# Kernel tuning notes

Measured on AMD Instinct MI355X. Metric: run time of the kernel, lower is better.

Reference implementation:

```python
import jax, jax.numpy as jnp
import numpy as np
import math

DIM = 512
HEADS = 8
DIM_HEAD = 64
SCALE = math.sqrt(DIM_HEAD)
EPS = 1e-12


def rms_norm(x, g):
    # F.normalize(x, dim=1) * g * sqrt(dim); x: [B, C, H, W], g: [C]
    inv = jax.lax.rsqrt(jnp.sum(x * x, axis=1, keepdims=True) + EPS)
    return x * inv * g[None, :, None, None] * jnp.asarray(math.sqrt(x.shape[1]), x.dtype)


def setup_inputs() -> dict:
    key = jax.random.key(0)
    k1, k2, k3 = jax.random.split(key, 3)
    B, H, W = 8, 64, 64
    hidden = HEADS * DIM_HEAD
    x = jax.random.normal(k1, (B, DIM, H, W), dtype=jnp.float32)
    w_qkv = jax.random.normal(k2, (3 * hidden, DIM), dtype=jnp.float32) * (1.0 / math.sqrt(DIM))
    w_out = jax.random.normal(k3, (DIM, hidden), dtype=jnp.float32) * (1.0 / math.sqrt(hidden))
    b_out = jnp.zeros((DIM,), dtype=jnp.float32)
    g1 = jnp.ones((DIM,), dtype=jnp.float32)
    g2 = jnp.ones((DIM,), dtype=jnp.float32)
    return {"x": x, "g1": g1, "w_qkv": w_qkv, "w_out": w_out, "b_out": b_out, "g2": g2}


def reference(x, g1, w_qkv, w_out, b_out, g2):
    B, C, H, W = x.shape
    n = H * W
    xn = rms_norm(x, g1)
    # 1x1 conv == channel matmul: [B, 3*hidden, H, W]
    qkv = jnp.einsum('bchw,oc->bohw', xn, w_qkv)
    q, k, v = jnp.split(qkv, 3, axis=1)
    # b (h c) x y -> b h c n
    def to_heads(t):
        return t.reshape(B, HEADS, DIM_HEAD, n)
    q, k, v = to_heads(q), to_heads(k), to_heads(v)
    q = jax.nn.softmax(q, axis=2) / SCALE   # softmax over channel dim d
    k = jax.nn.softmax(k, axis=3)           # softmax over spatial dim n
    context = jnp.einsum('bhdn,bhen->bhde', k, v)   # [B, H, d, e]
    out = jnp.einsum('bhde,bhdn->bhen', context, q) # [B, H, e, n]
    out = out.reshape(B, HEADS * DIM_HEAD, H, W)
    out = jnp.einsum('bchw,oc->bohw', out, w_out) + b_out[None, :, None, None]
    return rms_norm(out, g2)
```

## Files before the change

kernel.cpp:

```cpp
#include <hip/hip_runtime.h>


typedef unsigned short u16;
typedef __attribute__((ext_vector_type(8))) short short8;
typedef __attribute__((ext_vector_type(4))) short short4_t;
typedef __attribute__((ext_vector_type(4))) float f32x4;

static constexpr size_t XN_B = (size_t)512 * 4096;
static constexpr size_t KV_B = (size_t)1024 * 4096;
static constexpr float SQRT512 = 22.62741699796952f;

typedef const __attribute__((address_space(1))) unsigned int gu32;
typedef __attribute__((address_space(3))) unsigned int lu32;

__device__ __forceinline__ float b2f(u16 u){
  union { unsigned u; float f; } x; x.u = ((unsigned)u) << 16; return x.f;
}
__device__ __forceinline__ u16 f2b(float f){
  union { float f; unsigned u; } x; x.f = f;
  unsigned r = x.u + 0x7FFFu + ((x.u >> 16) & 1u);
  return (u16)(r >> 16);
}
__device__ __forceinline__ void gl16(const u16* g, u16* l){
  __builtin_amdgcn_global_load_lds((gu32*)g, (lu32*)l, 16, 0, 0);
}

__global__ __launch_bounds__(256)
void kprep(const float* __restrict__ wqkv, const float* __restrict__ wout,
           const float* __restrict__ g1, u16* __restrict__ dq, u16* __restrict__ dw,
           const float* __restrict__ x, u16* __restrict__ xnT,
           float* __restrict__ sden){
  __shared__ u16 lt[32][514];
  __shared__ float red4[256][4];
  __shared__ float invs[32];
  int bid = blockIdx.x;
  int t = threadIdx.x;
  if (bid < 1024){
    if (bid < 16) sden[bid * 256 + t] = 0.f;
    size_t i = ((size_t)bid * 256 + t) * 4;
    short4_t o;
    if (i < (size_t)786432){
      f32x4 v = *(const f32x4*)(wqkv + i);
      int c = (int)(i & 511);
      #pragma unroll
      for (int j = 0; j < 4; j++) o[j] = (short)f2b(v[j] * g1[c + j] * SQRT512);
      *(short4_t*)(dq + i) = o;
    } else {
      size_t off = i - 786432;
      f32x4 v = *(const f32x4*)(wout + off);
      #pragma unroll
      for (int j = 0; j < 4; j++) o[j] = (short)f2b(v[j]);
      *(short4_t*)(dw + off) = o;
    }
    return;
  }
  int pg0 = (bid - 1024) * 32;
  int b = pg0 >> 12, p0 = pg0 & 4095;
  int pxg = (t & 7) * 4;
  int chunk = t >> 3;
  const float* xp = x + (size_t)b * XN_B + p0 + pxg;
  f32x4 s = {0.f, 0.f, 0.f, 0.f};
  #pragma unroll 4
  for (int c = chunk * 16; c < chunk * 16 + 16; ++c){
    f32x4 v = *(const f32x4*)(xp + (size_t)c * 4096);
    #pragma unroll
    for (int j = 0; j < 4; j++){
      lt[pxg + j][c] = f2b(v[j]);
      s[j] += v[j] * v[j];
    }
  }
  *(f32x4*)red4[t] = s;
  __syncthreads();
  if (t < 32){
    int pg = t >> 2, pe = t & 3;
    float sum = 0.f;
    #pragma unroll
    for (int ch = 0; ch < 32; ch++) sum += red4[ch * 8 + pg][pe];
    invs[t] = rsqrtf(sum + 1e-12f);
  }
  __syncthreads();
  int px2 = t >> 3, c0 = (t & 7) * 8;
  float iv = invs[px2];
  u16* dst = xnT + (size_t)(pg0 + px2) * 512;
  #pragma unroll
  for (int j = 0; j < 8; j++){
    int c = c0 + j * 64;
    short8 o;
    #pragma unroll
    for (int e = 0; e < 8; e++) o[e] = (short)f2b(b2f(lt[px2][c + e]) * iv);
    *(short8*)(dst + c) = o;
  }
}

__global__ __launch_bounds__(256)
void gemm_qkv(const u16* __restrict__ Wkv, const u16* __restrict__ wq,
              const u16* __restrict__ xnT, u16* __restrict__ kvb,
              u16* __restrict__ qT)
{
  constexpr int NT = 8;
  const int bid = blockIdx.x;
  const u16* A; const u16* BT; u16* C;
  int m0, n0; size_t ldc; bool smax;
  if (bid < 2048){
    int ntile = bid & 31, mtile = (bid >> 5) & 7, z = bid >> 8;
    A = Wkv; BT = xnT + (size_t)z * XN_B; C = kvb + (size_t)z * KV_B;
    m0 = mtile * 128; n0 = ntile * 128; ldc = 4096; smax = false;
  } else {
    int idx = bid - 2048;
    int ntile = idx & 3, mtile = idx >> 2;
    A = xnT; BT = wq; C = qT;
    m0 = mtile * 128; n0 = ntile * 128; ldc = 512; smax = true;
  }
  __shared__ u16 As[2][128 * 64];
  __shared__ u16 Bs[2][128 * 64];
  const int tid = threadIdx.x;
  const int srow0 = tid >> 3;
  const int schunk = tid & 7;
  const int lane = tid & 63, wid = tid >> 6;
  const int wr = (wid >> 1) * 64, wc = (wid & 1) * 64;
  const int fr = lane & 15, fq = lane >> 4;
  f32x4 acc[4][4] = {};

  auto STAGE = [&](int s, int t){
    const int k0 = t * 64;
    #pragma unroll
    for (int r = 0; r < 4; r++){
      int row = r * 32 + srow0;
      int gj = (schunk ^ (row & 7)) * 8;
      gl16(A  + (size_t)(m0 + row) * 512 + k0 + gj, &As[s][0] + r * 2048 + tid * 8);
      gl16(BT + (size_t)(n0 + row) * 512 + k0 + gj, &Bs[s][0] + r * 2048 + tid * 8);
    }
  };

  STAGE(0, 0);
  int cur = 0;
  for (int t = 0; t < NT; t++){
    if (t + 1 < NT){
      STAGE(cur ^ 1, t + 1);
      asm volatile("s_waitcnt vmcnt(8)" ::: "memory");
    } else {
      asm volatile("s_waitcnt vmcnt(0)" ::: "memory");
    }
    __builtin_amdgcn_s_barrier();
    __builtin_amdgcn_sched_barrier(0);
    #pragma unroll
    for (int ks = 0; ks < 2; ks++){
      short8 a[4], b[4];
      #pragma unroll
      for (int i = 0; i < 4; i++){
        int ra = wr + i * 16 + fr;
        a[i] = *(const short8*)(&As[cur][0] + ra * 64 + ((ks * 4 + fq) ^ (ra & 7)) * 8);
        int rb = wc + i * 16 + fr;
        b[i] = *(const short8*)(&Bs[cur][0] + rb * 64 + ((ks * 4 + fq) ^ (rb & 7)) * 8);
      }
      #pragma unroll
      for (int i = 0; i < 4; i++)
        #pragma unroll
        for (int j = 0; j < 4; j++)
          acc[i][j] = __builtin_amdgcn_mfma_f32_16x16x32_bf16(a[i], b[j], acc[i][j], 0, 0, 0);
    }
    __builtin_amdgcn_sched_barrier(0);
    __builtin_amdgcn_s_barrier();
    cur ^= 1;
  }

  if (smax){
    #pragma unroll
    for (int i = 0; i < 4; i++)
      #pragma unroll
      for (int e = 0; e < 4; e++){
        float mx = fmaxf(fmaxf(acc[i][0][e], acc[i][1][e]),
                         fmaxf(acc[i][2][e], acc[i][3][e]));
        mx = fmaxf(mx, __shfl_xor(mx, 1));
        mx = fmaxf(mx, __shfl_xor(mx, 2));
        mx = fmaxf(mx, __shfl_xor(mx, 4));
        mx = fmaxf(mx, __shfl_xor(mx, 8));
        float p0 = __expf(acc[i][0][e] - mx);
        float p1 = __expf(acc[i][1][e] - mx);
        float p2 = __expf(acc[i][2][e] - mx);
        float p3 = __expf(acc[i][3][e] - mx);
        float s = p0 + p1 + p2 + p3;
        s += __shfl_xor(s, 1);
        s += __shfl_xor(s, 2);
        s += __shfl_xor(s, 4);
        s += __shfl_xor(s, 8);
        float r = 1.f / (s * 8.0f);
        acc[i][0][e] = p0 * r; acc[i][1][e] = p1 * r;
        acc[i][2][e] = p2 * r; acc[i][3][e] = p3 * r;
      }
  }
  #pragma unroll
  for (int i = 0; i < 4; i++)
    #pragma unroll
    for (int j = 0; j < 4; j++)
      #pragma unroll
      for (int e = 0; e < 4; e++){
        int row = m0 + wr + i * 16 + fq * 4 + e;
        int col = n0 + wc + j * 16 + fr;
        C[(size_t)row * ldc + col] = f2b(acc[i][j][e]);
      }
}

__global__ __launch_bounds__(256)
void gemm_out(const u16* __restrict__ qT, const u16* __restrict__ Mb,
              u16* __restrict__ out2T, const float* __restrict__ bias)
{
  constexpr int NT = 8;
  const int z = blockIdx.z;
  const u16* A  = qT + (size_t)z * 4096 * 512;
  const u16* BT = Mb + (size_t)z * 262144;
  u16* C = out2T + (size_t)z * 4096 * 512;
  const int m0 = blockIdx.y * 128, n0 = blockIdx.x * 128;
  __shared__ u16 As[2][128 * 64];
  __shared__ u16 Bs[2][128 * 64];
  const int tid = threadIdx.x;
  const int srow0 = tid >> 3;
  const int schunk = tid & 7;
  const int lane = tid & 63, wid = tid >> 6;
  const int wr = (wid >> 1) * 64, wc = (wid & 1) * 64;
  const int fr = lane & 15, fq = lane >> 4;
  f32x4 acc[4][4] = {};

  auto STAGE = [&](int s, int t){
    const int k0 = t * 64;
    #pragma unroll
    for (int r = 0; r < 4; r++){
      int row = r * 32 + srow0;
      int gj = (schunk ^ (row & 7)) * 8;
      gl16(A  + (size_t)(m0 + row) * 512 + k0 + gj, &As[s][0] + r * 2048 + tid * 8);
      gl16(BT + (size_t)(n0 + row) * 512 + k0 + gj, &Bs[s][0] + r * 2048 + tid * 8);
    }
  };

  STAGE(0, 0);
  int cur = 0;
  for (int t = 0; t < NT; t++){
    if (t + 1 < NT){
      STAGE(cur ^ 1, t + 1);
      asm volatile("s_waitcnt vmcnt(8)" ::: "memory");
    } else {
      asm volatile("s_waitcnt vmcnt(0)" ::: "memory");
    }
    __builtin_amdgcn_s_barrier();
    __builtin_amdgcn_sched_barrier(0);
    #pragma unroll
    for (int ks = 0; ks < 2; ks++){
      short8 a[4], b[4];
      #pragma unroll
      for (int i = 0; i < 4; i++){
        int ra = wr + i * 16 + fr;
        a[i] = *(const short8*)(&As[cur][0] + ra * 64 + ((ks * 4 + fq) ^ (ra & 7)) * 8);
        int rb = wc + i * 16 + fr;
        b[i] = *(const short8*)(&Bs[cur][0] + rb * 64 + ((ks * 4 + fq) ^ (rb & 7)) * 8);
      }
      #pragma unroll
      for (int i = 0; i < 4; i++)
        #pragma unroll
        for (int j = 0; j < 4; j++)
          acc[i][j] = __builtin_amdgcn_mfma_f32_16x16x32_bf16(a[i], b[j], acc[i][j], 0, 0, 0);
    }
    __builtin_amdgcn_sched_barrier(0);
    __builtin_amdgcn_s_barrier();
    cur ^= 1;
  }

  #pragma unroll
  for (int i = 0; i < 4; i++)
    #pragma unroll
    for (int j = 0; j < 4; j++)
      #pragma unroll
      for (int e = 0; e < 4; e++){
        int row = m0 + wr + i * 16 + fq * 4 + e;
        int col = n0 + wc + j * 16 + fr;
        C[(size_t)row * 512 + col] = f2b(acc[i][j][e] + bias[col]);
      }
}

__global__ __launch_bounds__(256)
void gemm_ctx(const u16* __restrict__ kv, float* __restrict__ P,
              float* __restrict__ sden)
{
  constexpr int K = 512;
  const int z = blockIdx.z;
  const int tid = threadIdx.x;
  const int ar = tid >> 2, ac = (tid & 3) * 8;
  int bh = z >> 3, sp = z & 7, b = bh >> 3, h = bh & 7;
  const u16* A  = kv + (size_t)b * KV_B + (size_t)(h * 64) * 4096 + sp * 512;
  const u16* BT = kv + (size_t)b * KV_B + (size_t)(512 + h * 64) * 4096 + sp * 512;
  __shared__ u16 As[64 * 40];
  __shared__ u16 Bs[64 * 40];
  const int wid = tid >> 6, lane = tid & 63;
  const int wr = (wid >> 1) * 32, wc = (wid & 1) * 32;
  const int lr = lane & 15, kb = lane >> 4;
  f32x4 acc[2][2] = {};
  float ssum = 0.f;
  for (int k0 = 0; k0 < K; k0 += 32){
    short8 av = *(const short8*)(A + (size_t)ar * 4096 + k0 + ac);
    short8 ao;
    #pragma unroll
    for (int e = 0; e < 8; e++){
      float ev = __expf(b2f((u16)av[e]));
      ao[e] = (short)f2b(ev);
      ssum += ev;
    }
    *(short8*)(As + ar * 40 + ac) = ao;
    *(short8*)(Bs + ar * 40 + ac) = *(const short8*)(BT + (size_t)ar * 4096 + k0 + ac);
    __syncthreads();
    short8 a0 = *(const short8*)(As + (wr +      lr) * 40 + kb * 8);
    short8 a1 = *(const short8*)(As + (wr + 16 + lr) * 40 + kb * 8);
    short8 b0 = *(const short8*)(Bs + (wc +      lr) * 40 + kb * 8);
    short8 b1 = *(const short8*)(Bs + (wc + 16 + lr) * 40 + kb * 8);
    acc[0][0] = __builtin_amdgcn_mfma_f32_16x16x32_bf16(a0, b0, acc[0][0], 0, 0, 0);
    acc[0][1] = __builtin_amdgcn_mfma_f32_16x16x32_bf16(a0, b1, acc[0][1], 0, 0, 0);
    acc[1][0] = __builtin_amdgcn_mfma_f32_16x16x32_bf16(a1, b0, acc[1][0], 0, 0, 0);
    acc[1][1] = __builtin_amdgcn_mfma_f32_16x16x32_bf16(a1, b1, acc[1][1], 0, 0, 0);
    __syncthreads();
  }
  ssum += __shfl_xor(ssum, 1);
  ssum += __shfl_xor(ssum, 2);
  if ((tid & 3) == 0) atomicAdd(sden + b * 512 + h * 64 + ar, ssum);
  #pragma unroll
  for (int mi = 0; mi < 2; mi++)
    #pragma unroll
    for (int ni = 0; ni < 2; ni++)
      #pragma unroll
      for (int j = 0; j < 4; j++){
        int row = wr + mi * 16 + kb * 4 + j;
        int col = wc + ni * 16 + lr;
        P[(size_t)z * 4096 + (size_t)row * 64 + col] = acc[mi][ni][j];
      }
}

__global__ __launch_bounds__(256)
void kctxw(const float* __restrict__ P, const float* __restrict__ sden,
           const u16* __restrict__ woutbf, u16* __restrict__ M)
{
  const int z = blockIdx.z;
  const int b = z >> 3, h = z & 7;
  const int m0 = blockIdx.y * 64;
  const int tid = threadIdx.x;
  __shared__ u16 As[64 * 72];
  __shared__ u16 Bs[64 * 72];
  {
    int r = tid >> 2, c0 = (tid & 3) * 16;
    const u16* wsrc = woutbf + (size_t)(m0 + r) * 512 + h * 64 + c0;
    *(short8*)(As + r * 72 + c0)     = *(const short8*)(wsrc);
    *(short8*)(As + r * 72 + c0 + 8) = *(const short8*)(wsrc + 8);
    float rs = 1.f / sden[b * 512 + h * 64 + r];
    const float* p = P + (size_t)z * 32768 + (size_t)r * 64 + c0;
    #pragma unroll
    for (int e = 0; e < 16; e++){
      float s = 0.f;
      #pragma unroll
      for (int sp = 0; sp < 8; sp++) s += p[e + sp * 4096];
      Bs[r * 72 + c0 + e] = f2b(s * rs);
    }
  }
  __syncthreads();
  const int wid = tid >> 6, lane = tid & 63;
  const int wr = (wid >> 1) * 32, wc = (wid & 1) * 32;
  const int lr = lane & 15, kb = lane >> 4;
  f32x4 acc[2][2] = {};
  #pragma unroll
  for (int k0 = 0; k0 < 64; k0 += 32){
    short8 a0 = *(const short8*)(As + (wr +      lr) * 72 + k0 + kb * 8);
    short8 a1 = *(const short8*)(As + (wr + 16 + lr) * 72 + k0 + kb * 8);
    short8 b0 = *(const short8*)(Bs + (wc +      lr) * 72 + k0 + kb * 8);
    short8 b1 = *(const short8*)(Bs + (wc + 16 + lr) * 72 + k0 + kb * 8);
    acc[0][0] = __builtin_amdgcn_mfma_f32_16x16x32_bf16(a0, b0, acc[0][0], 0, 0, 0);
    acc[0][1] = __builtin_amdgcn_mfma_f32_16x16x32_bf16(a0, b1, acc[0][1], 0, 0, 0);
    acc[1][0] = __builtin_amdgcn_mfma_f32_16x16x32_bf16(a1, b0, acc[1][0], 0, 0, 0);
    acc[1][1] = __builtin_amdgcn_mfma_f32_16x16x32_bf16(a1, b1, acc[1][1], 0, 0, 0);
  }
  #pragma unroll
  for (int mi = 0; mi < 2; mi++)
    #pragma unroll
    for (int ni = 0; ni < 2; ni++)
      #pragma unroll
      for (int j = 0; j < 4; j++){
        int row = m0 + wr + mi * 16 + kb * 4 + j;
        int col = wc + ni * 16 + lr;
        M[(size_t)b * 262144 + (size_t)row * 512 + h * 64 + col] = f2b(acc[mi][ni][j]);
      }
}

__global__ __launch_bounds__(256)
void krms2(const u16* __restrict__ o2, const float* __restrict__ g,
           float* __restrict__ out){
  __shared__ u16 lt[32][514];
  __shared__ float invs[32];
  __shared__ float gl[512];
  int t = threadIdx.x;
  int pg0 = blockIdx.x * 32;
  int b = pg0 >> 12, p0 = pg0 & 4095;
  gl[t] = g[t] * SQRT512;
  gl[t + 256] = g[t + 256] * SQRT512;
  int px2 = t >> 3, c0 = (t & 7) * 8;
  const u16* src = o2 + (size_t)(pg0 + px2) * 512;
  float s = 0.f;
  #pragma unroll
  for (int j = 0; j < 8; j++){
    int c = c0 + j * 64;
    short8 v = *(const short8*)(src + c);
    *(short8*)&lt[px2][c] = v;
    #pragma unroll
    for (int e = 0; e < 8; e++){ float f = b2f((u16)v[e]); s += f * f; }
  }
  s += __shfl_xor(s, 1); s += __shfl_xor(s, 2); s += __shfl_xor(s, 4);
  if ((t & 7) == 0) invs[px2] = rsqrtf(s + 1e-12f);
  __syncthreads();
  int c2 = t >> 2, pxc = (t & 3) * 8;
  float ivv[8];
  #pragma unroll
  for (int e = 0; e < 8; e++) ivv[e] = invs[pxc + e];
  #pragma unroll
  for (int pass = 0; pass < 8; pass++){
    int c = c2 + pass * 64;
    float gf = gl[c];
    float* dst = out + ((size_t)(b * 512 + c)) * 4096 + p0 + pxc;
    #pragma unroll
    for (int q = 0; q < 2; q++){
      f32x4 o;
      #pragma unroll
      for (int e = 0; e < 4; e++){
        int pp = q * 4 + e;
        o[e] = b2f(lt[pxc + pp][c]) * ivv[pp] * gf;
      }
      *(f32x4*)(dst + q * 4) = o;
    }
  }
}

extern "C" void kernel_launch(void* const* d_in, const int* in_sizes, int n_in,
                              void* d_out, int out_size, void* d_ws, size_t ws_size,
                              hipStream_t stream)
{
  (void)in_sizes; (void)n_in; (void)out_size; (void)ws_size;
  const float* x    = (const float*)d_in[0];
  const float* g1   = (const float*)d_in[1];
  const float* wqkv = (const float*)d_in[2];
  const float* wout = (const float*)d_in[3];
  const float* bout = (const float*)d_in[4];
  const float* g2   = (const float*)d_in[5];
  float* out = (float*)d_out;
  char* ws = (char*)d_ws;

  u16*   xnT   = (u16*)(ws);
  float* P     = (float*)(ws);
  u16*   M     = (u16*)(ws + (size_t)8388608);
  u16*   qT    = (u16*)(ws + (size_t)33554432);
  u16*   kv    = (u16*)(ws + (size_t)67108864);
  u16*   out2T = (u16*)(ws + (size_t)67108864);
  u16*   wbf   = (u16*)(ws + (size_t)134217728);
  u16*   wkvbf = wbf + (size_t)512 * 512;
  u16*   woutbf= (u16*)(ws + (size_t)135790592);
  float* sden  = (float*)(ws + (size_t)136314880);

  kprep<<<2048, 256, 0, stream>>>(wqkv, wout, g1, wbf, woutbf, x, xnT, sden);
  gemm_qkv<<<3072, 256, 0, stream>>>(wkvbf, wbf, xnT, kv, qT);
  gemm_ctx<<<dim3(1, 1, 512), 256, 0, stream>>>(kv, P, sden);
  kctxw<<<dim3(1, 8, 64), 256, 0, stream>>>(P, sden, woutbf, M);
  gemm_out<<<dim3(4, 32, 8), 256, 0, stream>>>(qT, M, out2T, bout);
  krms2<<<1024, 256, 0, stream>>>(out2T, g2, out);
}
```

Before: 177.9 us.

## Fuse output projection GEMM with final RMS norm and transposed store

The output GEMM now gives each 512-thread block all 512 output channels for a 128-pixel tile. This lets it compute the per-pixel RMS norm in registers via shuffles and LDS, then transpose through LDS to write the final fp32 NCHW output directly. It removes the bf16 intermediate write/read and the separate krms2 launch. In exchange the grid drops to 256 blocks with more registers per thread (4x8 accumulators) and a smaller K-step of 32, which may lower occupancy and latency hiding.

Measured after the change: 163.8 us, median of 2. -8.0%, faster.

```diff
diff --git a/kernel.cpp b/kernel.cpp
--- a/kernel.cpp
+++ b/kernel.cpp
@@ -201,34 +201,43 @@
       }
 }
 
-__global__ __launch_bounds__(256)
-void gemm_out(const u16* __restrict__ qT, const u16* __restrict__ Mb,
-              u16* __restrict__ out2T, const float* __restrict__ bias)
+__global__ __launch_bounds__(512)
+void gemm_outrms(const u16* __restrict__ qT, const u16* __restrict__ Mb,
+                 const float* __restrict__ bias, const float* __restrict__ g2,
+                 float* __restrict__ out)
 {
-  constexpr int NT = 8;
-  const int z = blockIdx.z;
+  constexpr int NT = 16;
+  const int mt = blockIdx.x, z = blockIdx.y;
   const u16* A  = qT + (size_t)z * 4096 * 512;
   const u16* BT = Mb + (size_t)z * 262144;
-  u16* C = out2T + (size_t)z * 4096 * 512;
-  const int m0 = blockIdx.y * 128, n0 = blockIdx.x * 128;
-  __shared__ u16 As[2][128 * 64];
-  __shared__ u16 Bs[2][128 * 64];
+  const int m0 = mt * 128;
+
+  __shared__ char smem[84480] __attribute__((aligned(16)));
+  u16*   As    = (u16*)smem;
+  u16*   Bs    = (u16*)(smem + 16384);
+  float* trans = (float*)smem;
+  float* rsum  = (float*)(smem + 81920);
+  float* invr  = (float*)(smem + 83968);
+
   const int tid = threadIdx.x;
-  const int srow0 = tid >> 3;
-  const int schunk = tid & 7;
   const int lane = tid & 63, wid = tid >> 6;
-  const int wr = (wid >> 1) * 64, wc = (wid & 1) * 64;
+  const int wr = (wid >> 2) * 64;
+  const int wc = (wid & 3) * 128;
   const int fr = lane & 15, fq = lane >> 4;
-  f32x4 acc[4][4] = {};
+  const int srow = tid >> 2, schunk = tid & 3;
+  f32x4 acc[4][8] = {};
 
   auto STAGE = [&](int s, int t){
-    const int k0 = t * 64;
+    const int k0 = t * 32;
+    {
+      int gj = (schunk ^ ((srow >> 1) & 3)) * 8;
+      gl16(A + (size_t)(m0 + srow) * 512 + k0 + gj, As + s * 4096 + tid * 8);
+    }
     #pragma unroll
     for (int r = 0; r < 4; r++){
-      int row = r * 32 + srow0;
-      int gj = (schunk ^ (row & 7)) * 8;
-      gl16(A  + (size_t)(m0 + row) * 512 + k0 + gj, &As[s][0] + r * 2048 + tid * 8);
-      gl16(BT + (size_t)(n0 + row) * 512 + k0 + gj, &Bs[s][0] + r * 2048 + tid * 8);
+      int row = r * 128 + srow;
+      int gj = (schunk ^ ((row >> 1) & 3)) * 8;
+      gl16(BT + (size_t)row * 512 + k0 + gj, Bs + s * 16384 + r * 4096 + tid * 8);
     }
   };
 
@@ -237,43 +246,94 @@
   for (int t = 0; t < NT; t++){
     if (t + 1 < NT){
       STAGE(cur ^ 1, t + 1);
-      asm volatile("s_waitcnt vmcnt(8)" ::: "memory");
+      asm volatile("s_waitcnt vmcnt(5)" ::: "memory");
     } else {
       asm volatile("s_waitcnt vmcnt(0)" ::: "memory");
     }
     __builtin_amdgcn_s_barrier();
     __builtin_amdgcn_sched_barrier(0);
-    #pragma unroll
-    for (int ks = 0; ks < 2; ks++){
-      short8 a[4], b[4];
-      #pragma unroll
-      for (int i = 0; i < 4; i++){
-        int ra = wr + i * 16 + fr;
-        a[i] = *(const short8*)(&As[cur][0] + ra * 64 + ((ks * 4 + fq) ^ (ra & 7)) * 8);
-        int rb = wc + i * 16 + fr;
-        b[i] = *(const short8*)(&Bs[cur][0] + rb * 64 + ((ks * 4 + fq) ^ (rb & 7)) * 8);
-      }
-      #pragma unroll
-      for (int i = 0; i < 4; i++)
-        #pragma unroll
-        for (int j = 0; j < 4; j++)
-          acc[i][j] = __builtin_amdgcn_mfma_f32_16x16x32_bf16(a[i], b[j], acc[i][j], 0, 0, 0);
-    }
+    short8 a[4], b[8];
+    #pragma unroll
+    for (int i = 0; i < 4; i++){
+      int ra = wr + i * 16 + fr;
+      a[i] = *(const short8*)(As + cur * 4096 + ra * 32 + ((fq ^ ((ra >> 1) & 3)) * 8));
+    }
+    #pragma unroll
+    for (int j = 0; j < 8; j++){
+      int rb = wc + j * 16 + fr;
+      b[j] = *(const short8*)(Bs + cur * 16384 + rb * 32 + ((fq ^ ((rb >> 1) & 3)) * 8));
+    }
+    #pragma unroll
+    for (int i = 0; i < 4; i++)
+      #pragma unroll
+      for (int j = 0; j < 8; j++)
+        acc[i][j] = __builtin_amdgcn_mfma_f32_16x16x32_bf16(a[i], b[j], acc[i][j], 0, 0, 0);
     __builtin_amdgcn_sched_barrier(0);
     __builtin_amdgcn_s_barrier();
     cur ^= 1;
   }
 
+  float bcol[8], gcol[8];
+  #pragma unroll
+  for (int j = 0; j < 8; j++){
+    int col = wc + j * 16 + fr;
+    bcol[j] = bias[col];
+    gcol[j] = g2[col] * SQRT512;
+  }
   #pragma unroll
   for (int i = 0; i < 4; i++)
     #pragma unroll
-    for (int j = 0; j < 4; j++)
-      #pragma unroll
-      for (int e = 0; e < 4; e++){
-        int row = m0 + wr + i * 16 + fq * 4 + e;
-        int col = n0 + wc + j * 16 + fr;
-        C[(size_t)row * 512 + col] = f2b(acc[i][j][e] + bias[col]);
-      }
+    for (int e = 0; e < 4; e++){
+      float p = 0.f;
+      #pragma unroll
+      for (int j = 0; j < 8; j++){
+        acc[i][j][e] += bcol[j];
+        p += acc[i][j][e] * acc[i][j][e];
+      }
+      p += __shfl_xor(p, 1); p += __shfl_xor(p, 2);
+      p += __shfl_xor(p, 4); p += __shfl_xor(p, 8);
+      if (fr == 0) rsum[(wr + i * 16 + fq * 4 + e) * 4 + (wid & 3)] = p;
+    }
+  __syncthreads();
+  if (tid < 128){
+    float ss = rsum[tid * 4] + rsum[tid * 4 + 1] + rsum[tid * 4 + 2] + rsum[tid * 4 + 3];
+    invr[tid] = rsqrtf(ss + 1e-12f);
+  }
+  __syncthreads();
+  #pragma unroll
+  for (int i = 0; i < 4; i++)
+    #pragma unroll
+    for (int e = 0; e < 4; e++){
+      float iv = invr[wr + i * 16 + fq * 4 + e];
+      #pragma unroll
+      for (int j = 0; j < 8; j++)
+        acc[i][j][e] *= iv * gcol[j];
+    }
+  const int myhalf = wid >> 2;
+  const int cbase = tid >> 3, pi = (tid & 7) * 4;
+  #pragma unroll
+  for (int q = 0; q < 4; q++){
+    __syncthreads();
+    if (myhalf == (q >> 1)){
+      #pragma unroll
+      for (int ii = 0; ii < 2; ii++){
+        const int i = (q & 1) * 2 + ii;
+        const int ro = ii * 16 + fq * 4;
+        #pragma unroll
+        for (int j = 0; j < 8; j++){
+          int col = wc + j * 16 + fr;
+          *(f32x4*)&trans[col * 40 + ro] = acc[i][j];
+        }
+      }
+    }
+    __syncthreads();
+    #pragma unroll
+    for (int it = 0; it < 8; it++){
+      int cc = it * 64 + cbase;
+      f32x4 v = *(const f32x4*)&trans[cc * 40 + pi];
+      *(f32x4*)(out + ((size_t)(z * 512 + cc)) * 4096 + m0 + q * 32 + pi) = v;
+    }
+  }
 }
 
 __global__ __launch_bounds__(256)
@@ -384,53 +444,6 @@
       }
 }
 
-__global__ __launch_bounds__(256)
-void krms2(const u16* __restrict__ o2, const float* __restrict__ g,
-           float* __restrict__ out){
-  __shared__ u16 lt[32][514];
-  __shared__ float invs[32];
-  __shared__ float gl[512];
-  int t = threadIdx.x;
-  int pg0 = blockIdx.x * 32;
-  int b = pg0 >> 12, p0 = pg0 & 4095;
-  gl[t] = g[t] * SQRT512;
-  gl[t + 256] = g[t + 256] * SQRT512;
-  int px2 = t >> 3, c0 = (t & 7) * 8;
-  const u16* src = o2 + (size_t)(pg0 + px2) * 512;
-  float s = 0.f;
-  #pragma unroll
-  for (int j = 0; j < 8; j++){
-    int c = c0 + j * 64;
-    short8 v = *(const short8*)(src + c);
-    *(short8*)&lt[px2][c] = v;
-    #pragma unroll
-    for (int e = 0; e < 8; e++){ float f = b2f((u16)v[e]); s += f * f; }
-  }
-  s += __shfl_xor(s, 1); s += __shfl_xor(s, 2); s += __shfl_xor(s, 4);
-  if ((t & 7) == 0) invs[px2] = rsqrtf(s + 1e-12f);
-  __syncthreads();
-  int c2 = t >> 2, pxc = (t & 3) * 8;
-  float ivv[8];
-  #pragma unroll
-  for (int e = 0; e < 8; e++) ivv[e] = invs[pxc + e];
-  #pragma unroll
-  for (int pass = 0; pass < 8; pass++){
-    int c = c2 + pass * 64;
-    float gf = gl[c];
-    float* dst = out + ((size_t)(b * 512 + c)) * 4096 + p0 + pxc;
-    #pragma unroll
-    for (int q = 0; q < 2; q++){
-      f32x4 o;
-      #pragma unroll
-      for (int e = 0; e < 4; e++){
-        int pp = q * 4 + e;
-        o[e] = b2f(lt[pxc + pp][c]) * ivv[pp] * gf;
-      }
-      *(f32x4*)(dst + q * 4) = o;
-    }
-  }
-}
-
 extern "C" void kernel_launch(void* const* d_in, const int* in_sizes, int n_in,
                               void* d_out, int out_size, void* d_ws, size_t ws_size,
                               hipStream_t stream)
@@ -450,7 +463,6 @@
   u16*   M     = (u16*)(ws + (size_t)8388608);
   u16*   qT    = (u16*)(ws + (size_t)33554432);
   u16*   kv    = (u16*)(ws + (size_t)67108864);
-  u16*   out2T = (u16*)(ws + (size_t)67108864);
   u16*   wbf   = (u16*)(ws + (size_t)134217728);
   u16*   wkvbf = wbf + (size_t)512 * 512;
   u16*   woutbf= (u16*)(ws + (size_t)135790592);
@@ -460,6 +472,5 @@
   gemm_qkv<<<3072, 256, 0, stream>>>(wkvbf, wbf, xnT, kv, qT);
   gemm_ctx<<<dim3(1, 1, 512), 256, 0, stream>>>(kv, P, sden);
   kctxw<<<dim3(1, 8, 64), 256, 0, stream>>>(P, sden, woutbf, M);
-  gemm_out<<<dim3(4, 32, 8), 256, 0, stream>>>(qT, M, out2T, bout);
-  krms2<<<1024, 256, 0, stream>>>(out2T, g2, out);
-}
+  gemm_outrms<<<dim3(32, 8), 512, 0, stream>>>(qT, M, bout, g2, out);
+}
```
